# Kernel optimization log

Measured on AMD Instinct MI355X. Metric: run time of the kernel, lower is better.

## Reference

```python
import jax, jax.numpy as jnp
import numpy as np

N = 16384
IN_FEATS = 256
OUT_FEATS = 256


def setup_inputs() -> dict:
    key = jax.random.key(0)
    k1, k2, k3, k4 = jax.random.split(key, 4)
    # dense (row-normalized-ish) adjacency; scaled so aggregated values stay O(1)
    graph = jax.random.uniform(k1, (N, N), dtype=jnp.float32) / N
    features = jax.random.normal(k2, (N, IN_FEATS), dtype=jnp.float32)
    # nn.Linear params: W [out, in], b [out]
    W = jax.random.normal(k3, (OUT_FEATS, IN_FEATS), dtype=jnp.float32) / np.sqrt(IN_FEATS)
    b = jax.random.normal(k4, (OUT_FEATS,), dtype=jnp.float32) * 0.01
    return {"graph": graph, "features": features, "W": W, "b": b}


def reference(graph, features, W, b):
    # h = graph @ features  (GCN-style dense neighbor aggregation)
    h = jnp.matmul(graph, features)            # [N, in_feats]
    # linear: h @ W.T + b
    h = jnp.einsum('ni,oi->no', h, W) + b      # [N, out_feats]
    # activation = relu (norm = None)
    return jax.nn.relu(h)
```

## Files before the change

kernel.cpp:

```cpp
#include <hip/hip_runtime.h>
#include <hip/hip_bf16.h>

typedef float f32x4 __attribute__((ext_vector_type(4)));
typedef short short8 __attribute__((ext_vector_type(8)));
typedef __bf16 bf16x8 __attribute__((ext_vector_type(8)));

#define N_TOT 16384
#define FEATS 256
#define BM 256
#define BK 32
#define KSPLIT 4
#define NSTEPS ((N_TOT / KSPLIT) / BK)
#define LDSA_BYTES (BM * 128)
#define LDSB_BYTES (FEATS * 64)
#define TILE_BYTES (LDSA_BYTES + LDSB_BYTES)

static __device__ __forceinline__ ushort f2bf(float f) {
  union { __hip_bfloat16 b; ushort u; } cv;
  cv.b = __float2bfloat16(f);
  return cv.u;
}
static __device__ __forceinline__ float bf2f(ushort u) {
  union { unsigned int i; float f; } c;
  c.i = ((unsigned int)u) << 16;
  return c.f;
}
static __device__ __forceinline__ void gload_lds16(const void* g, void* l) {
  __builtin_amdgcn_global_load_lds((const __attribute__((address_space(1))) unsigned int*)g,
                                   (__attribute__((address_space(3))) unsigned int*)l,
                                   16, 0, 0);
}

__global__ __launch_bounds__(256) void k_transpose(const float* __restrict__ feat,
                                                   ushort* __restrict__ fT) {
  __shared__ float tile[64][65];
  const int tx = threadIdx.x & 63, ty = threadIdx.x >> 6;
  const int k0 = blockIdx.x * 64, n0 = blockIdx.y * 64;
#pragma unroll
  for (int j = 0; j < 64; j += 4)
    tile[ty + j][tx] = feat[(size_t)(k0 + ty + j) * FEATS + n0 + tx];
  __syncthreads();
#pragma unroll
  for (int j = 0; j < 64; j += 4)
    fT[(size_t)(n0 + ty + j) * N_TOT + k0 + tx] = f2bf(tile[tx][ty + j]);
}

__global__ __launch_bounds__(256) void k_convw(const float* __restrict__ W,
                                               ushort* __restrict__ Wb) {
  int i = (blockIdx.x * 256 + threadIdx.x) * 4;
  float4 v = *(const float4*)(W + i);
  ushort4 h = { f2bf(v.x), f2bf(v.y), f2bf(v.z), f2bf(v.w) };
  *(ushort4*)(Wb + i) = h;
}

__global__ __launch_bounds__(512, 2) void k_gemm1(const float* __restrict__ graph,
                                                  const ushort* __restrict__ fT,
                                                  ushort* __restrict__ parts) {
  __shared__ char lds[3][TILE_BYTES];
  const int tid = threadIdx.x;
  const int lane = tid & 63, w = tid >> 6;
  const int wm = w >> 2, wn = w & 3;
  const size_t m0 = (size_t)blockIdx.x * BM;
  const int kbase = blockIdx.y * (N_TOT / KSPLIT);

  auto stage = [&](int bf, int t) {
    const int k0 = kbase + t * BK;
    char* ldsA = &lds[bf][0];
    char* ldsB = &lds[bf][LDSA_BYTES];
#pragma unroll
    for (int j = 0; j < 4; ++j) {
      const int r0 = w * 32 + j * 8;
      const int row = r0 + (lane >> 3);
      const int c = (lane & 7) ^ (row & 7);
      gload_lds16(graph + (m0 + row) * (size_t)N_TOT + k0 + c * 4, ldsA + r0 * 128);
    }
#pragma unroll
    for (int j = 0; j < 2; ++j) {
      const int r0 = w * 32 + j * 16;
      const int row = r0 + (lane >> 2);
      const int c = (lane & 3) ^ (row & 3);
      gload_lds16(fT + (size_t)row * N_TOT + k0 + c * 8, ldsB + r0 * 64);
    }
  };

  f32x4 acc[8][4] = {};
  const int rsel = lane & 15;
  const int kg = lane >> 4;

  auto compute = [&](int bf) {
    const char* Ab = &lds[bf][0];
    const char* Bb = &lds[bf][LDSA_BYTES];
    short8 bfr[4];
#pragma unroll
    for (int nf = 0; nf < 4; ++nf) {
      const int row = wn * 64 + nf * 16 + rsel;
      const int c = kg ^ (row & 3);
      bfr[nf] = *(const short8*)(Bb + row * 64 + c * 16);
    }
#pragma unroll
    for (int mf = 0; mf < 8; ++mf) {
      const int row = wm * 128 + mf * 16 + rsel;
      const int cb = (row & 7);
      const float4 a0 = *(const float4*)(Ab + row * 128 + ((kg * 2) ^ cb) * 16);
      const float4 a1 = *(const float4*)(Ab + row * 128 + ((kg * 2 + 1) ^ cb) * 16);
      short8 af = { (short)f2bf(a0.x), (short)f2bf(a0.y), (short)f2bf(a0.z), (short)f2bf(a0.w),
                    (short)f2bf(a1.x), (short)f2bf(a1.y), (short)f2bf(a1.z), (short)f2bf(a1.w) };
#pragma unroll
      for (int nf = 0; nf < 4; ++nf)
        acc[mf][nf] = __builtin_amdgcn_mfma_f32_16x16x32_bf16(
            __builtin_bit_cast(bf16x8, af), __builtin_bit_cast(bf16x8, bfr[nf]),
            acc[mf][nf], 0, 0, 0);
    }
  };

  stage(0, 0);
  stage(1, 1);
  stage(2, 2);

  for (int t = 0; t < NSTEPS - 2; ++t) {
    asm volatile("s_waitcnt vmcnt(12)" ::: "memory");
    __builtin_amdgcn_s_barrier();
    compute(t % 3);
    __builtin_amdgcn_s_barrier();
    __builtin_amdgcn_sched_barrier(0);
    if (t + 3 < NSTEPS) stage(t % 3, t + 3);
  }
  asm volatile("s_waitcnt vmcnt(6)" ::: "memory");
  __builtin_amdgcn_s_barrier();
  compute((NSTEPS - 2) % 3);
  asm volatile("s_waitcnt vmcnt(0)" ::: "memory");
  __builtin_amdgcn_s_barrier();
  compute((NSTEPS - 1) % 3);

  ushort* p = parts + (size_t)blockIdx.y * N_TOT * FEATS;
#pragma unroll
  for (int mf = 0; mf < 8; ++mf)
#pragma unroll
    for (int nf = 0; nf < 4; ++nf)
#pragma unroll
      for (int j = 0; j < 4; ++j) {
        const int row = wm * 128 + mf * 16 + ((lane >> 4) << 2) + j;
        const int col = wn * 64 + nf * 16 + (lane & 15);
        p[(m0 + row) * FEATS + col] = f2bf(acc[mf][nf][j]);
      }
}

__global__ __launch_bounds__(256) void k_gemm2(const ushort* __restrict__ parts,
                                               const ushort* __restrict__ Wb,
                                               const float* __restrict__ bias,
                                               float* __restrict__ out) {
  __shared__ ushort Al[64][264];
  __shared__ ushort Bl[FEATS][40];
  const int tid = threadIdx.x;
  const int lane = tid & 63, w = tid >> 6;
  const size_t m0 = (size_t)blockIdx.x * 64;

  for (int c = tid; c < 2048; c += 256) {
    const int row = c >> 5;
    const int k8 = (c & 31) << 3;
    const size_t off = (m0 + row) * FEATS + k8;
    float s[8] = {0, 0, 0, 0, 0, 0, 0, 0};
#pragma unroll
    for (int p = 0; p < KSPLIT; ++p) {
      const short8 v = *(const short8*)(parts + (size_t)p * N_TOT * FEATS + off);
#pragma unroll
      for (int j = 0; j < 8; ++j) s[j] += bf2f((ushort)v[j]);
    }
    short8 ov;
#pragma unroll
    for (int j = 0; j < 8; ++j) ov[j] = (short)f2bf(s[j]);
    *(short8*)&Al[row][k8] = ov;
  }

  f32x4 acc[16] = {};
  for (int kk = 0; kk < FEATS; kk += 32) {
    __syncthreads();
#pragma unroll
    for (int q = 0; q < 4; ++q) {
      const short8 v = *(const short8*)(Wb + (size_t)tid * FEATS + kk + q * 8);
      *(short8*)&Bl[tid][q * 8] = v;
    }
    __syncthreads();
    const int koff = (lane >> 4) << 3;
    const short8 af = *(const short8*)&Al[w * 16 + (lane & 15)][kk + koff];
#pragma unroll
    for (int nf = 0; nf < 16; ++nf) {
      const short8 bfv = *(const short8*)&Bl[nf * 16 + (lane & 15)][koff];
      acc[nf] = __builtin_amdgcn_mfma_f32_16x16x32_bf16(
          __builtin_bit_cast(bf16x8, af), __builtin_bit_cast(bf16x8, bfv),
          acc[nf], 0, 0, 0);
    }
  }

#pragma unroll
  for (int nf = 0; nf < 16; ++nf) {
    const int col = nf * 16 + (lane & 15);
    const float bc = bias[col];
#pragma unroll
    for (int j = 0; j < 4; ++j) {
      const int row = w * 16 + ((lane >> 4) << 2) + j;
      const float v = acc[nf][j] + bc;
      out[(m0 + row) * FEATS + col] = fmaxf(v, 0.0f);
    }
  }
}

extern "C" void kernel_launch(void* const* d_in, const int* in_sizes, int n_in,
                              void* d_out, int out_size, void* d_ws, size_t ws_size,
                              hipStream_t stream) {
  const float* graph = (const float*)d_in[0];
  const float* feat  = (const float*)d_in[1];
  const float* W     = (const float*)d_in[2];
  const float* bias  = (const float*)d_in[3];
  float* out = (float*)d_out;

  char* ws = (char*)d_ws;
  ushort* fT    = (ushort*)ws;
  ushort* Wb    = (ushort*)(ws + (size_t)8 * 1024 * 1024);
  ushort* parts = (ushort*)(ws + (size_t)8 * 1024 * 1024 + 131072);

  k_transpose<<<dim3(N_TOT / 64, FEATS / 64), 256, 0, stream>>>(feat, fT);
  k_convw<<<dim3(64), 256, 0, stream>>>(W, Wb);
  k_gemm1<<<dim3(N_TOT / BM, KSPLIT), 512, 0, stream>>>(graph, fT, parts);
  k_gemm2<<<dim3(N_TOT / 64), 256, 0, stream>>>(parts, Wb, bias, out);
}
```

Measured before the change: 319.4 us.

## Halve GEMM1 row tile, double-buffer, remap blocks per XCD, stagger K start

Shrinks the first GEMM's row tile from 256 to 128 and drops from triple to double buffering, so more blocks fit per CU (launch bound raised to 4). Blocks are launched on a 1D grid and remapped so blocks on the same XCD share a K-split slice and its feature panel in L2. Each block also starts its K loop at a staggered phase offset to spread DRAM traffic across channels. The cost is less reuse of the B tile per A row, shallower prefetch, and more register and LDS pressure from running more blocks at once.

```diff
diff --git a/kernel.cpp b/kernel.cpp
--- a/kernel.cpp
+++ b/kernel.cpp
@@ -7,7 +7,7 @@
 
 #define N_TOT 16384
 #define FEATS 256
-#define BM 256
+#define BM 128
 #define BK 32
 #define KSPLIT 4
 #define NSTEPS ((N_TOT / KSPLIT) / BK)
@@ -53,23 +53,29 @@
   *(ushort4*)(Wb + i) = h;
 }
 
-__global__ __launch_bounds__(512, 2) void k_gemm1(const float* __restrict__ graph,
+__global__ __launch_bounds__(512, 4) void k_gemm1(const float* __restrict__ graph,
                                                   const ushort* __restrict__ fT,
                                                   ushort* __restrict__ parts) {
-  __shared__ char lds[3][TILE_BYTES];
+  __shared__ char lds[2][TILE_BYTES];
   const int tid = threadIdx.x;
   const int lane = tid & 63, w = tid >> 6;
   const int wm = w >> 2, wn = w & 3;
-  const size_t m0 = (size_t)blockIdx.x * BM;
-  const int kbase = blockIdx.y * (N_TOT / KSPLIT);
+
+  const int b = blockIdx.x;
+  const int xcd = b & 7;
+  const int kb = xcd >> 1;
+  const int mi = (b >> 3) | ((xcd & 1) << 6);
+  const size_t m0 = (size_t)mi * BM;
+  const int kbase = kb * (N_TOT / KSPLIT);
+  const int ph = (b * 53) & (NSTEPS - 1);
 
   auto stage = [&](int bf, int t) {
     const int k0 = kbase + t * BK;
     char* ldsA = &lds[bf][0];
     char* ldsB = &lds[bf][LDSA_BYTES];
 #pragma unroll
-    for (int j = 0; j < 4; ++j) {
-      const int r0 = w * 32 + j * 8;
+    for (int j = 0; j < 2; ++j) {
+      const int r0 = w * 16 + j * 8;
       const int row = r0 + (lane >> 3);
       const int c = (lane & 7) ^ (row & 7);
       gload_lds16(graph + (m0 + row) * (size_t)N_TOT + k0 + c * 4, ldsA + r0 * 128);
@@ -83,7 +89,7 @@
     }
   };
 
-  f32x4 acc[8][4] = {};
+  f32x4 acc[4][4] = {};
   const int rsel = lane & 15;
   const int kg = lane >> 4;
 
@@ -98,8 +104,8 @@
       bfr[nf] = *(const short8*)(Bb + row * 64 + c * 16);
     }
 #pragma unroll
-    for (int mf = 0; mf < 8; ++mf) {
-      const int row = wm * 128 + mf * 16 + rsel;
+    for (int mf = 0; mf < 4; ++mf) {
+      const int row = wm * 64 + mf * 16 + rsel;
       const int cb = (row & 7);
       const float4 a0 = *(const float4*)(Ab + row * 128 + ((kg * 2) ^ cb) * 16);
       const float4 a1 = *(const float4*)(Ab + row * 128 + ((kg * 2 + 1) ^ cb) * 16);
@@ -113,33 +119,34 @@
     }
   };
 
-  stage(0, 0);
-  stage(1, 1);
-  stage(2, 2);
-
-  for (int t = 0; t < NSTEPS - 2; ++t) {
-    asm volatile("s_waitcnt vmcnt(12)" ::: "memory");
-    __builtin_amdgcn_s_barrier();
-    compute(t % 3);
+  stage(0, ph);
+  stage(1, (ph + 1) & (NSTEPS - 1));
+
+  for (int s = 0; s < NSTEPS - 2; ++s) {
+    asm volatile("s_waitcnt vmcnt(4)" ::: "memory");
     __builtin_amdgcn_s_barrier();
     __builtin_amdgcn_sched_barrier(0);
-    if (t + 3 < NSTEPS) stage(t % 3, t + 3);
-  }
-  asm volatile("s_waitcnt vmcnt(6)" ::: "memory");
+    compute(s & 1);
+    __builtin_amdgcn_s_barrier();
+    stage(s & 1, (s + 2 + ph) & (NSTEPS - 1));
+  }
+  asm volatile("s_waitcnt vmcnt(4)" ::: "memory");
   __builtin_amdgcn_s_barrier();
-  compute((NSTEPS - 2) % 3);
+  __builtin_amdgcn_sched_barrier(0);
+  compute((NSTEPS - 2) & 1);
   asm volatile("s_waitcnt vmcnt(0)" ::: "memory");
   __builtin_amdgcn_s_barrier();
-  compute((NSTEPS - 1) % 3);
-
-  ushort* p = parts + (size_t)blockIdx.y * N_TOT * FEATS;
-#pragma unroll
-  for (int mf = 0; mf < 8; ++mf)
+  __builtin_amdgcn_sched_barrier(0);
+  compute((NSTEPS - 1) & 1);
+
+  ushort* p = parts + (size_t)kb * N_TOT * FEATS;
+#pragma unroll
+  for (int mf = 0; mf < 4; ++mf)
 #pragma unroll
     for (int nf = 0; nf < 4; ++nf)
 #pragma unroll
       for (int j = 0; j < 4; ++j) {
-        const int row = wm * 128 + mf * 16 + ((lane >> 4) << 2) + j;
+        const int row = wm * 64 + mf * 16 + ((lane >> 4) << 2) + j;
         const int col = wn * 64 + nf * 16 + (lane & 15);
         p[(m0 + row) * FEATS + col] = f2bf(acc[mf][nf][j]);
       }
@@ -221,6 +228,6 @@
 
   k_transpose<<<dim3(N_TOT / 64, FEATS / 64), 256, 0, stream>>>(feat, fT);
   k_convw<<<dim3(64), 256, 0, stream>>>(W, Wb);
-  k_gemm1<<<dim3(N_TOT / BM, KSPLIT), 512, 0, stream>>>(graph, fT, parts);
+  k_gemm1<<<dim3((N_TOT / BM) * KSPLIT), 512, 0, stream>>>(graph, fT, parts);
   k_gemm2<<<dim3(N_TOT / 64), 256, 0, stream>>>(parts, Wb, bias, out);
 }
```

Result: faster. 282.7 us (-11.5%).
